# Optimization experiments

Measured on AMD Instinct MI355X. Metric: run time of the kernel, lower is better.

## Reference

```python
import jax, jax.numpy as jnp
import numpy as np

D_MODEL = 512
N_HEADS = 16
D_HEAD = D_MODEL // N_HEADS


def _relative_shift(pos_score):
    # pos_score: [B, H, T, T]  (Transformer-XL shift trick)
    B, H, T1, T2 = pos_score.shape
    padded = jnp.pad(pos_score, ((0, 0), (0, 0), (0, 0), (1, 0)))  # [B,H,T1,T2+1]
    padded = padded.reshape(B, H, T2 + 1, T1)
    return padded[:, :, 1:].reshape(B, H, T1, T2)


def setup_inputs() -> dict:
    key = jax.random.key(0)
    ks = jax.random.split(key, 12)
    B, T, D = 4, 1024, D_MODEL
    s = 1.0 / np.sqrt(D)
    return {
        "q": jax.random.normal(ks[0], (B, T, D), jnp.float32),
        "k": jax.random.normal(ks[1], (B, T, D), jnp.float32),
        "v": jax.random.normal(ks[2], (B, T, D), jnp.float32),
        "pos_embedding": jax.random.normal(ks[3], (B, T, D), jnp.float32),
        "Wq": jax.random.normal(ks[4], (D, D), jnp.float32) * s,
        "bq": jnp.zeros((D,), jnp.float32),
        "Wp": jax.random.normal(ks[5], (D, D), jnp.float32) * s,
        "Wf": jax.random.normal(ks[6], (D, D), jnp.float32) * s,
        "bf": jnp.zeros((D,), jnp.float32),
        "u_bias": jax.random.normal(ks[7], (N_HEADS, D_HEAD), jnp.float32) * s,
        "v_bias": jax.random.normal(ks[8], (N_HEADS, D_HEAD), jnp.float32) * s,
    }


def reference(q, k, v, pos_embedding, Wq, bq, Wp, Wf, bf, u_bias, v_bias):
    B, T, D = q.shape
    H, Dh = N_HEADS, D_HEAD
    sqrt_dim = jnp.asarray(np.sqrt(D_MODEL), q.dtype)
    # NOTE: original module uses linear_q for q, k AND v (faithful to source)
    qh = (q @ Wq + bq).reshape(B, T, H, Dh)            # [B,T,H,Dh]
    kh = (k @ Wq + bq).reshape(B, T, H, Dh)
    vh = (v @ Wq + bq).reshape(B, T, H, Dh)
    ph = (pos_embedding @ Wp).reshape(B, T, H, Dh)     # no bias

    content_score = jnp.einsum('bthd,bshd->bhts', qh + u_bias, kh)
    pos_score = jnp.einsum('bthd,bshd->bhts', qh + v_bias, ph)
    pos_score = _relative_shift(pos_score)

    score = (content_score + pos_score) / sqrt_dim     # [B,H,T,T]
    attn = jax.nn.softmax(score, axis=-1)              # dropout identity in eval
    context = jnp.einsum('bhts,bshd->bthd', attn, vh).reshape(B, T, D)
    return context @ Wf + bf
```

## Files before the change

### kernel.cpp

```cpp
#include <hip/hip_runtime.h>
#include <hip/hip_bf16.h>

typedef __bf16 bf16;
typedef bf16 bf16x8 __attribute__((ext_vector_type(8)));
typedef bf16 bf16x4 __attribute__((ext_vector_type(4)));
typedef float f32x4 __attribute__((ext_vector_type(4)));

#define SCALE_LOG2 0.06376237f


__global__ __launch_bounds__(256) void prep_kernel(
    const float* __restrict__ Wq, const float* __restrict__ Wp, const float* __restrict__ Wf,
    bf16* __restrict__ WqT, bf16* __restrict__ WpT, bf16* __restrict__ WfT)
{
  const int tid = threadIdx.x;
  __shared__ bf16 t[64][72];
  const int m = blockIdx.x >> 6;
  const int tb = blockIdx.x & 63;
  const int tr = tb >> 3, tc = tb & 7;
  const float* W = (m == 0) ? Wq : (m == 1) ? Wp : Wf;
  bf16*        O = (m == 0) ? WqT : (m == 1) ? WpT : WfT;
  const int r = tid >> 2, cg = tid & 3;
  {
    const float* src = W + (size_t)(tr * 64 + r) * 512 + tc * 64 + cg * 16;
    f32x4 a = *(const f32x4*)src, b2 = *(const f32x4*)(src + 4);
    f32x4 c = *(const f32x4*)(src + 8), d = *(const f32x4*)(src + 12);
    bf16x8 lo, hi;
#pragma unroll
    for (int j = 0; j < 4; j++) { lo[j] = (bf16)a[j]; lo[4 + j] = (bf16)b2[j]; hi[j] = (bf16)c[j]; hi[4 + j] = (bf16)d[j]; }
    *(bf16x8*)(&t[r][cg * 16])     = lo;
    *(bf16x8*)(&t[r][cg * 16 + 8]) = hi;
  }
  __syncthreads();
  bf16x8 o0, o1;
#pragma unroll
  for (int j = 0; j < 8; j++) { o0[j] = t[cg * 16 + j][r]; o1[j] = t[cg * 16 + 8 + j][r]; }
  bf16* dst = O + (size_t)(tc * 64 + r) * 512 + tr * 64 + cg * 16;
  *(bf16x8*)dst = o0;
  *(bf16x8*)(dst + 8) = o1;
}

__global__ __launch_bounds__(256) void proj_gemm(
    const float* __restrict__ q, const float* __restrict__ k, const float* __restrict__ v,
    const float* __restrict__ pos,
    const bf16* __restrict__ WqT, const bf16* __restrict__ WpT, const float* __restrict__ bq,
    bf16* __restrict__ qh, bf16* __restrict__ kh, bf16* __restrict__ vT, bf16* __restrict__ phx)
{
  __shared__ float Asf[128 * 68];
  __shared__ bf16  Bs[128 * 72];
  const int tid = threadIdx.x;
  const int wave = tid >> 6, lane = tid & 63, quad = lane >> 4, ln = lane & 15;
  const int tn = blockIdx.x & 3;
  const int tm = blockIdx.x >> 2;
  const int kind = tm >> 5;
  const int rr0 = (tm & 31) * 128;
  const float* X = (kind == 0) ? q : (kind == 1) ? k : (kind == 2) ? v : pos;
  const bf16* WT = ((kind < 3) ? WqT : WpT) + (size_t)tn * 128 * 512;
  const int qn_ = (wave & 1) * 64;
  const int qr_ = (wave >> 1) * 64;
  const int srow = tid >> 2, scg = tid & 3;

  f32x4 acc[4][4] = {};

  for (int kk = 0; kk < 8; kk++) {
    const int k0 = kk * 64;
    {
      const float* p0 = X + (size_t)(rr0 + srow) * 512 + k0 + scg * 16;
      const float* p1 = X + (size_t)(rr0 + srow + 64) * 512 + k0 + scg * 16;
#pragma unroll
      for (int u = 0; u < 4; u++) {
        *(f32x4*)(Asf + srow * 68 + scg * 16 + u * 4)        = *(const f32x4*)(p0 + u * 4);
        *(f32x4*)(Asf + (srow + 64) * 68 + scg * 16 + u * 4) = *(const f32x4*)(p1 + u * 4);
      }
      const bf16* w0 = WT + (size_t)srow * 512 + k0 + scg * 16;
      const bf16* w1 = WT + (size_t)(srow + 64) * 512 + k0 + scg * 16;
      *(bf16x8*)(Bs + srow * 72 + scg * 16)            = *(const bf16x8*)w0;
      *(bf16x8*)(Bs + srow * 72 + scg * 16 + 8)        = *(const bf16x8*)(w0 + 8);
      *(bf16x8*)(Bs + (srow + 64) * 72 + scg * 16)     = *(const bf16x8*)w1;
      *(bf16x8*)(Bs + (srow + 64) * 72 + scg * 16 + 8) = *(const bf16x8*)(w1 + 8);
    }
    __syncthreads();
#pragma unroll
    for (int ks = 0; ks < 2; ks++) {
      bf16x8 wf[4], xf[4];
#pragma unroll
      for (int i = 0; i < 4; i++) {
        wf[i] = *(const bf16x8*)(Bs + (qn_ + i * 16 + ln) * 72 + ks * 32 + quad * 8);
        f32x4 lo = *(const f32x4*)(Asf + (qr_ + i * 16 + ln) * 68 + ks * 32 + quad * 8);
        f32x4 hi = *(const f32x4*)(Asf + (qr_ + i * 16 + ln) * 68 + ks * 32 + quad * 8 + 4);
        bf16x8 t;
#pragma unroll
        for (int j = 0; j < 4; j++) { t[j] = (bf16)lo[j]; t[4 + j] = (bf16)hi[j]; }
        xf[i] = t;
      }
#pragma unroll
      for (int i = 0; i < 4; i++)
#pragma unroll
        for (int j = 0; j < 4; j++)
          acc[i][j] = __builtin_amdgcn_mfma_f32_16x16x32_bf16(wf[i], xf[j], acc[i][j], 0, 0, 0);
    }
    __syncthreads();
  }

#pragma unroll
  for (int i = 0; i < 4; i++) {
    const int nn0 = tn * 128 + qn_ + i * 16 + quad * 4;
    const int dd0 = nn0 & 31, hh = nn0 >> 5;
    f32x4 b4 = {0.f, 0.f, 0.f, 0.f};
    if (kind < 3) b4 = *(const f32x4*)(bq + nn0);
#pragma unroll
    for (int j = 0; j < 4; j++) {
      const int rr = rr0 + qr_ + j * 16 + ln;
      const int bb = rr >> 10, tt = rr & 1023;
      const size_t base = (size_t)(bb * 16 + hh);
      bf16x4 pk;
#pragma unroll
      for (int r = 0; r < 4; r++) pk[r] = (bf16)(acc[i][j][r] + b4[r]);
      if (kind == 0)      *(bf16x4*)(qh + (base * 1024 + tt) * 32 + dd0) = pk;
      else if (kind == 1) *(bf16x4*)(kh + (base * 1024 + tt) * 32 + dd0) = pk;
      else if (kind == 2) {
#pragma unroll
        for (int r = 0; r < 4; r++) vT[(base * 32 + dd0 + r) * 1024 + tt] = pk[r];
      } else {
        *(bf16x4*)(phx + (base * 2048 + tt) * 32 + dd0) = pk;
        if (tt <= 1021) *(bf16x4*)(phx + (base * 2048 + tt + 1025) * 32 + dd0) = pk;
        if (tt == 1023) {
          bf16x4 zz = {};
          *(bf16x4*)(phx + (base * 2048 + 1024) * 32 + dd0) = zz;
          *(bf16x4*)(phx + (base * 2048 + 2047) * 32 + dd0) = zz;
        }
      }
    }
  }
}

__global__ __launch_bounds__(256, 4) void attn_kernel(
    const bf16* __restrict__ qh, const bf16* __restrict__ kh,
    const bf16* __restrict__ vT, const bf16* __restrict__ phx,
    const float* __restrict__ u_bias, const float* __restrict__ v_bias,
    bf16* __restrict__ ctx)
{
  __shared__ float fs[4 * 16 * 84];
  __shared__ bf16  pb[4 * 16 * 72];

  const int tid = threadIdx.x;
  const int wave = tid >> 6, lane = tid & 63, quad = lane >> 4, ln = lane & 15;
  const int wg = blockIdx.x;
  const int bh = wg & 63, tq = wg >> 6;
  const int h = bh & 15, b = bh >> 4;
  const int t0 = tq * 64;
  const bf16* qh_h  = qh  + (size_t)bh * 1024 * 32;
  const bf16* kh_h  = kh  + (size_t)bh * 1024 * 32;
  const bf16* vT_h  = vT  + (size_t)bh * 32 * 1024;
  const bf16* phx_h = phx + (size_t)bh * 2048 * 32;

  float* fsw = fs + wave * 16 * 84;
  bf16*  pbw = pb + wave * 16 * 72;

  bf16x8 qu, qva, qvn;
  {
    const int t = t0 + wave * 16 + ln;
    bf16x8 q0 = *(const bf16x8*)(qh_h + (size_t)t * 32 + quad * 8);
    bf16x8 q1 = *(const bf16x8*)(qh_h + (size_t)(t + 1) * 32 + quad * 8);
    const float* ubp = u_bias + h * 32 + quad * 8;
    const float* vbp = v_bias + h * 32 + quad * 8;
#pragma unroll
    for (int j = 0; j < 8; j++) {
      qu[j]  = (bf16)(((float)q0[j] + ubp[j]) * SCALE_LOG2);
      qva[j] = (bf16)(((float)q0[j] + vbp[j]) * SCALE_LOG2);
      qvn[j] = (bf16)(((float)q1[j] + vbp[j]) * SCALE_LOG2);
    }
  }

  f32x4 O0 = {0.f, 0.f, 0.f, 0.f}, O1 = {0.f, 0.f, 0.f, 0.f};
  float l_lane = 0.0f;
  const f32x4 zf = {0.f, 0.f, 0.f, 0.f};

#pragma unroll 2
  for (int si = 0; si < 16; si++) {
    const int s0 = si * 64;
    const int jb0 = s0 - t0 + 960 + (3 - wave) * 16;

#pragma unroll
    for (int i = 0; i < 5; i++) {
      bf16x8 pbf = *(const bf16x8*)(phx_h + (size_t)(jb0 + i * 16 + ln) * 32 + quad * 8);
      bf16x8 bsel = (jb0 + i * 16 >= 1024) ? qvn : qva;
      f32x4 f = __builtin_amdgcn_mfma_f32_16x16x32_bf16(pbf, bsel, zf, 0, 0, 0);
      *(f32x4*)(fsw + ln * 84 + i * 16 + quad * 4) = f;
    }

    f32x4 c[4];
#pragma unroll
    for (int cs = 0; cs < 4; cs++) {
      bf16x8 kbf = *(const bf16x8*)(kh_h + (size_t)(s0 + cs * 16 + ln) * 32 + quad * 8);
      c[cs] = __builtin_amdgcn_mfma_f32_16x16x32_bf16(kbf, qu, zf, 0, 0, 0);
    }

#pragma unroll
    for (int cs = 0; cs < 4; cs++) {
      bf16x4 pk;
#pragma unroll
      for (int r = 0; r < 4; r++) {
        const int col = cs * 16 + quad * 4 + r - ln + 15;
        const float p = exp2f(c[cs][r] + fsw[ln * 84 + col]);
        l_lane += p;
        pk[r] = (bf16)p;
      }
      *(bf16x4*)(pbw + ln * 72 + cs * 16 + quad * 4) = pk;
    }

#pragma unroll
    for (int kb = 0; kb < 2; kb++) {
      bf16x8 a  = *(const bf16x8*)(pbw + ln * 72 + kb * 32 + quad * 8);
      bf16x8 b0 = *(const bf16x8*)(vT_h + (size_t)ln * 1024 + s0 + kb * 32 + quad * 8);
      bf16x8 b1 = *(const bf16x8*)(vT_h + (size_t)(16 + ln) * 1024 + s0 + kb * 32 + quad * 8);
      O0 = __builtin_amdgcn_mfma_f32_16x16x32_bf16(a, b0, O0, 0, 0, 0);
      O1 = __builtin_amdgcn_mfma_f32_16x16x32_bf16(a, b1, O1, 0, 0, 0);
    }
  }

  l_lane += __shfl_xor(l_lane, 16);
  l_lane += __shfl_xor(l_lane, 32);
#pragma unroll
  for (int r = 0; r < 4; r++) {
    const float lr = __shfl(l_lane, quad * 4 + r);
    const float inv = 1.0f / lr;
    const int t = t0 + wave * 16 + quad * 4 + r;
    const size_t o = ((size_t)(b * 1024 + t)) * 512 + h * 32;
    ctx[o + ln]      = (bf16)(O0[r] * inv);
    ctx[o + 16 + ln] = (bf16)(O1[r] * inv);
  }
}

__global__ __launch_bounds__(256) void out_gemm(
    const bf16* __restrict__ ctx, const bf16* __restrict__ WfT, const float* __restrict__ bfv,
    float* __restrict__ out)
{
  __shared__ bf16 As[64 * 40];
  __shared__ bf16 Bs[128 * 40];
  const int tid = threadIdx.x;
  const int wave = tid >> 6, lane = tid & 63, quad = lane >> 4, ln = lane & 15;
  const int tn = blockIdx.x & 3;
  const int tm = blockIdx.x >> 2;
  const int rr0 = tm * 64;
  const bf16* WT = WfT + (size_t)tn * 128 * 512;
  const int qm = (wave & 1) * 32, qn = (wave >> 1) * 64;
  const int srow = tid >> 2, scg = tid & 3;

  f32x4 acc[2][4] = {};
  for (int kk = 0; kk < 16; kk++) {
    const int k0 = kk * 32;
    *(bf16x8*)(As + srow * 40 + scg * 8)        = *(const bf16x8*)(ctx + (size_t)(rr0 + srow) * 512 + k0 + scg * 8);
    *(bf16x8*)(Bs + srow * 40 + scg * 8)        = *(const bf16x8*)(WT + (size_t)srow * 512 + k0 + scg * 8);
    *(bf16x8*)(Bs + (srow + 64) * 40 + scg * 8) = *(const bf16x8*)(WT + (size_t)(srow + 64) * 512 + k0 + scg * 8);
    __syncthreads();
    bf16x8 af[2], bfm[4];
#pragma unroll
    for (int i = 0; i < 2; i++)
      af[i] = *(const bf16x8*)(As + (qm + i * 16 + ln) * 40 + quad * 8);
#pragma unroll
    for (int j = 0; j < 4; j++)
      bfm[j] = *(const bf16x8*)(Bs + (qn + j * 16 + ln) * 40 + quad * 8);
#pragma unroll
    for (int i = 0; i < 2; i++)
#pragma unroll
      for (int j = 0; j < 4; j++)
        acc[i][j] = __builtin_amdgcn_mfma_f32_16x16x32_bf16(af[i], bfm[j], acc[i][j], 0, 0, 0);
    __syncthreads();
  }

#pragma unroll
  for (int i = 0; i < 2; i++)
#pragma unroll
    for (int j = 0; j < 4; j++) {
      const int nn = tn * 128 + qn + j * 16 + ln;
      const float bias = bfv[nn];
#pragma unroll
      for (int r = 0; r < 4; r++) {
        const int rr = rr0 + qm + i * 16 + quad * 4 + r;
        out[(size_t)rr * 512 + nn] = acc[i][j][r] + bias;
      }
    }
}

extern "C" void kernel_launch(void* const* d_in, const int* in_sizes, int n_in,
                              void* d_out, int out_size, void* d_ws, size_t ws_size,
                              hipStream_t stream) {
  const float* q   = (const float*)d_in[0];
  const float* k   = (const float*)d_in[1];
  const float* v   = (const float*)d_in[2];
  const float* pe  = (const float*)d_in[3];
  const float* Wq  = (const float*)d_in[4];
  const float* bq  = (const float*)d_in[5];
  const float* Wp  = (const float*)d_in[6];
  const float* Wf  = (const float*)d_in[7];
  const float* bfv = (const float*)d_in[8];
  const float* ub  = (const float*)d_in[9];
  const float* vb  = (const float*)d_in[10];

  bf16* ws  = (bf16*)d_ws;
  bf16* qh  = ws;
  bf16* kh  = qh + 2097152;
  bf16* vT  = kh + 2097152;
  bf16* phx = vT + 2097152;
  bf16* ctx = phx + 4194304;
  bf16* WqT = ctx + 2097152;
  bf16* WpT = WqT + 262144;
  bf16* WfT = WpT + 262144;

  prep_kernel<<<192, 256, 0, stream>>>(Wq, Wp, Wf, WqT, WpT, WfT);
  proj_gemm<<<512, 256, 0, stream>>>(q, k, v, pe, WqT, WpT, bq, qh, kh, vT, phx);
  attn_kernel<<<1024, 256, 0, stream>>>(qh, kh, vT, phx, ub, vb, ctx);
  out_gemm<<<256, 256, 0, stream>>>(ctx, WfT, bfv, (float*)d_out);
}
```

Measured before the change: 189.9 us.

## Split attention key range across two blocks and merge partials in output GEMM

The attention kernel now splits the key/sequence dimension into two halves, launching twice as many workgroups. Each writes unnormalized fp32 partial outputs and row sums, and the output projection GEMM combines them and normalizes while loading the A tile. No running max is used, so the two halves add directly. The exp2 call is also swapped for the hardware builtin. The cost is extra fp32 partial traffic (two 8 MB buffers written and read) and more work in the GEMM loader.

Result: slower. 201.6 us (+6.2%).

```diff
diff --git a/kernel.cpp b/kernel.cpp
--- a/kernel.cpp
+++ b/kernel.cpp
@@ -138,7 +138,8 @@
     const bf16* __restrict__ qh, const bf16* __restrict__ kh,
     const bf16* __restrict__ vT, const bf16* __restrict__ phx,
     const float* __restrict__ u_bias, const float* __restrict__ v_bias,
-    bf16* __restrict__ ctx)
+    float* __restrict__ Oa, float* __restrict__ Ob,
+    float* __restrict__ la, float* __restrict__ lb)
 {
   __shared__ float fs[4 * 16 * 84];
   __shared__ bf16  pb[4 * 16 * 72];
@@ -146,7 +147,9 @@
   const int tid = threadIdx.x;
   const int wave = tid >> 6, lane = tid & 63, quad = lane >> 4, ln = lane & 15;
   const int wg = blockIdx.x;
-  const int bh = wg & 63, tq = wg >> 6;
+  const int bh = wg & 63;
+  const int rest = wg >> 6;
+  const int tq = rest & 15, sc = rest >> 4;
   const int h = bh & 15, b = bh >> 4;
   const int t0 = tq * 64;
   const bf16* qh_h  = qh  + (size_t)bh * 1024 * 32;
@@ -176,8 +179,9 @@
   float l_lane = 0.0f;
   const f32x4 zf = {0.f, 0.f, 0.f, 0.f};
 
+  const int si0 = sc * 8;
 #pragma unroll 2
-  for (int si = 0; si < 16; si++) {
+  for (int si = si0; si < si0 + 8; si++) {
     const int s0 = si * 64;
     const int jb0 = s0 - t0 + 960 + (3 - wave) * 16;
 
@@ -202,7 +206,7 @@
 #pragma unroll
       for (int r = 0; r < 4; r++) {
         const int col = cs * 16 + quad * 4 + r - ln + 15;
-        const float p = exp2f(c[cs][r] + fsw[ln * 84 + col]);
+        const float p = __builtin_amdgcn_exp2f(c[cs][r] + fsw[ln * 84 + col]);
         l_lane += p;
         pk[r] = (bf16)p;
       }
@@ -221,23 +225,28 @@
 
   l_lane += __shfl_xor(l_lane, 16);
   l_lane += __shfl_xor(l_lane, 32);
+
+  float* Op = sc ? Ob : Oa;
+  float* lp = sc ? lb : la;
 #pragma unroll
   for (int r = 0; r < 4; r++) {
-    const float lr = __shfl(l_lane, quad * 4 + r);
-    const float inv = 1.0f / lr;
     const int t = t0 + wave * 16 + quad * 4 + r;
     const size_t o = ((size_t)(b * 1024 + t)) * 512 + h * 32;
-    ctx[o + ln]      = (bf16)(O0[r] * inv);
-    ctx[o + 16 + ln] = (bf16)(O1[r] * inv);
-  }
+    Op[o + ln]      = O0[r];
+    Op[o + 16 + ln] = O1[r];
+  }
+  if (lane < 16) lp[(size_t)bh * 1024 + t0 + wave * 16 + lane] = l_lane;
 }
 
 __global__ __launch_bounds__(256) void out_gemm(
-    const bf16* __restrict__ ctx, const bf16* __restrict__ WfT, const float* __restrict__ bfv,
+    const float* __restrict__ Oa, const float* __restrict__ Ob,
+    const float* __restrict__ la, const float* __restrict__ lb,
+    const bf16* __restrict__ WfT, const float* __restrict__ bfv,
     float* __restrict__ out)
 {
   __shared__ bf16 As[64 * 40];
   __shared__ bf16 Bs[128 * 40];
+  __shared__ float linv[16 * 64];
   const int tid = threadIdx.x;
   const int wave = tid >> 6, lane = tid & 63, quad = lane >> 4, ln = lane & 15;
   const int tn = blockIdx.x & 3;
@@ -247,10 +256,32 @@
   const int qm = (wave & 1) * 32, qn = (wave >> 1) * 64;
   const int srow = tid >> 2, scg = tid & 3;
 
+  for (int e = tid; e < 1024; e += 256) {
+    const int hh = e >> 6, r = e & 63;
+    const int row = rr0 + r;
+    const int b_ = row >> 10, t_ = row & 1023;
+    const size_t li = ((size_t)(b_ * 16 + hh)) * 1024 + t_;
+    linv[e] = 1.0f / (la[li] + lb[li]);
+  }
+  __syncthreads();
+
   f32x4 acc[2][4] = {};
   for (int kk = 0; kk < 16; kk++) {
     const int k0 = kk * 32;
-    *(bf16x8*)(As + srow * 40 + scg * 8)        = *(const bf16x8*)(ctx + (size_t)(rr0 + srow) * 512 + k0 + scg * 8);
+    {
+      const float* pa = Oa + (size_t)(rr0 + srow) * 512 + k0 + scg * 8;
+      const float* pcb = Ob + (size_t)(rr0 + srow) * 512 + k0 + scg * 8;
+      f32x4 a0 = *(const f32x4*)pa,  a1 = *(const f32x4*)(pa + 4);
+      f32x4 c0 = *(const f32x4*)pcb, c1 = *(const f32x4*)(pcb + 4);
+      const float s = linv[kk * 64 + srow];
+      bf16x8 t8;
+#pragma unroll
+      for (int j = 0; j < 4; j++) {
+        t8[j]     = (bf16)((a0[j] + c0[j]) * s);
+        t8[4 + j] = (bf16)((a1[j] + c1[j]) * s);
+      }
+      *(bf16x8*)(As + srow * 40 + scg * 8) = t8;
+    }
     *(bf16x8*)(Bs + srow * 40 + scg * 8)        = *(const bf16x8*)(WT + (size_t)srow * 512 + k0 + scg * 8);
     *(bf16x8*)(Bs + (srow + 64) * 40 + scg * 8) = *(const bf16x8*)(WT + (size_t)(srow + 64) * 512 + k0 + scg * 8);
     __syncthreads();
@@ -303,13 +334,16 @@
   bf16* kh  = qh + 2097152;
   bf16* vT  = kh + 2097152;
   bf16* phx = vT + 2097152;
-  bf16* ctx = phx + 4194304;
-  bf16* WqT = ctx + 2097152;
+  bf16* WqT = phx + 4194304;
   bf16* WpT = WqT + 262144;
   bf16* WfT = WpT + 262144;
+  float* Oa = (float*)(WfT + 262144);
+  float* Ob = Oa + 2097152;
+  float* la = Ob + 2097152;
+  float* lb = la + 65536;
 
   prep_kernel<<<192, 256, 0, stream>>>(Wq, Wp, Wf, WqT, WpT, WfT);
   proj_gemm<<<512, 256, 0, stream>>>(q, k, v, pe, WqT, WpT, bq, qh, kh, vT, phx);
-  attn_kernel<<<1024, 256, 0, stream>>>(qh, kh, vT, phx, ub, vb, ctx);
-  out_gemm<<<256, 256, 0, stream>>>(ctx, WfT, bfv, (float*)d_out);
-}
+  attn_kernel<<<2048, 256, 0, stream>>>(qh, kh, vT, phx, ub, vb, Oa, Ob, la, lb);
+  out_gemm<<<256, 256, 0, stream>>>(Oa, Ob, la, lb, WfT, bfv, (float*)d_out);
+}
```
